# Kernel optimization log

Measured on AMD Instinct MI355X. Metric: run time of the kernel, lower is better.

Reference implementation:

```python
import jax, jax.numpy as jnp
import numpy as np
from jax import lax

N_T, N_CAPS, CAP_DIM = 8, 16, 16
EPS = 1e-6


def setup_inputs() -> dict:
    key = jax.random.key(0)
    k1, k2 = jax.random.split(key)
    B, H, W = 4, 64, 64
    C = N_T * N_CAPS * CAP_DIM  # 2048
    z = jax.random.normal(k1, (B, C, H, W), dtype=jnp.float32)
    u = jax.random.normal(k2, (B, C, H, W), dtype=jnp.float32)
    weight = jnp.ones((1, 1, 3, 3, 1), dtype=jnp.float32)  # Conv3d (O,I,kT,kD,kS), init ones
    beta = jnp.ones((1,), dtype=jnp.float32)  # correlated_mean_beta, mu_init=1.0
    return {"z": z, "u": u, "weight": weight, "beta": beta}


def reference(z, u, weight, beta):
    B, C, H, W = u.shape
    hw = H * W
    # (B, n_t, n_caps, cap_dim, hw) -> (B, n_caps, n_t, cap_dim, hw) -> (B*n_caps, 1, n_t, cap_dim, hw)
    u_caps = u.reshape(B, N_T, N_CAPS, CAP_DIM, hw)
    u_caps = jnp.transpose(u_caps, (0, 2, 1, 3, 4))
    u_caps = u_caps.reshape(-1, 1, N_T, CAP_DIM, hw)
    u_sq = u_caps * u_caps
    # circular pad over transform and cap_dim axes to keep 'same' size with 3x3x1 kernel
    padded = jnp.pad(u_sq, ((0, 0), (0, 0), (1, 1), (1, 1), (0, 0)), mode="wrap")
    v = lax.conv_general_dilated(
        padded, weight, window_strides=(1, 1, 1), padding="VALID",
        dimension_numbers=("NCDHW", "OIDHW", "NCDHW"),
    )  # (B*n_caps, 1, n_t, cap_dim, hw)
    v = v.reshape(B, N_CAPS, N_T, CAP_DIM, hw)
    v = jnp.transpose(v, (0, 2, 1, 3, 4)).reshape(z.shape)
    std = lax.rsqrt(v + EPS)
    s = (z + beta) * std
    return s
```

## Files before the change

### kernel.cpp

```cpp
#include <hip/hip_runtime.h>

#define N_T 8
#define N_CAPS 16
#define CAP_DIM 16
#define HW 4096
#define P_TILE 64
#define EPS 1e-6f

__global__ __launch_bounds__(256) void caps_norm_kernel(
    const float* __restrict__ z, const float* __restrict__ u,
    const float* __restrict__ w, const float* __restrict__ beta,
    float* __restrict__ out)
{
    __shared__ float lds[128 * P_TILE];

    const int tid = threadIdx.x;
    const int bid = blockIdx.x;
    const int ptile = bid & 63;
    const int c     = (bid >> 6) & 15;
    const int b     = bid >> 10;
    const int p0    = ptile * P_TILE;

    float W9[9];
#pragma unroll
    for (int i = 0; i < 9; ++i) W9[i] = w[i];
    const float bet = beta[0];

    const size_t base_b = (size_t)b * 2048 * HW;

#pragma unroll
    for (int k = 0; k < 8; ++k) {
        int s = tid + k * 256;
        int r = s >> 4;
        int q = s & 15;
        int t = r >> 4, d = r & 15;
        int ch = t * 256 + c * 16 + d;
        const float4 v = *(const float4*)(u + base_b + (size_t)ch * HW + p0 + q * 4);
        float4 sq;
        sq.x = v.x * v.x; sq.y = v.y * v.y; sq.z = v.z * v.z; sq.w = v.w * v.w;
        *(float4*)(lds + r * P_TILE + q * 4) = sq;
    }
    __syncthreads();

    const float4* L = (const float4*)lds;

#pragma unroll
    for (int k = 0; k < 8; ++k) {
        int s = tid + k * 256;
        int r = s >> 4;
        int q = s & 15;
        int t = r >> 4, d = r & 15;

        float ax = 0.f, ay = 0.f, az = 0.f, aw = 0.f;
#pragma unroll
        for (int i = 0; i < 3; ++i) {
            int tt = (t + i + 7) & 7;
#pragma unroll
            for (int j = 0; j < 3; ++j) {
                int dd = (d + j + 15) & 15;
                float ww = W9[i * 3 + j];
                float4 a = L[((tt << 4) + dd) * 16 + q];
                ax += ww * a.x; ay += ww * a.y; az += ww * a.z; aw += ww * a.w;
            }
        }

        int ch = t * 256 + c * 16 + d;
        size_t gidx = base_b + (size_t)ch * HW + p0 + q * 4;
        const float4 z4 = *(const float4*)(z + gidx);
        float4 o;
        o.x = (z4.x + bet) * rsqrtf(ax + EPS);
        o.y = (z4.y + bet) * rsqrtf(ay + EPS);
        o.z = (z4.z + bet) * rsqrtf(az + EPS);
        o.w = (z4.w + bet) * rsqrtf(aw + EPS);
        *(float4*)(out + gidx) = o;
    }
}

extern "C" void kernel_launch(void* const* d_in, const int* in_sizes, int n_in,
                              void* d_out, int out_size, void* d_ws, size_t ws_size,
                              hipStream_t stream) {
    const float* z    = (const float*)d_in[0];
    const float* u    = (const float*)d_in[1];
    const float* w    = (const float*)d_in[2];
    const float* beta = (const float*)d_in[3];
    float* out = (float*)d_out;

    caps_norm_kernel<<<dim3(4096), dim3(256), 0, stream>>>(z, u, w, beta, out);
}
```

Measured before the change: 317.7 us.

## Double-buffer LDS and prefetch next tile across four tiles per block

Each block now processes four consecutive pixel tiles instead of one. The u and z loads for the next tile are issued before computing the current tile, and the squared values go into alternating LDS buffers. The aim is to overlap global memory latency with the stencil compute and to amortise the per-block setup. In exchange the grid shrinks by four, LDS use per block doubles and register pressure rises, which can reduce occupancy.

After: 321.2 us. About the same (+1.1%).

```diff
diff --git a/kernel.cpp b/kernel.cpp
--- a/kernel.cpp
+++ b/kernel.cpp
@@ -5,21 +5,22 @@
 #define CAP_DIM 16
 #define HW 4096
 #define P_TILE 64
+#define NTILES 4
 #define EPS 1e-6f
 
-__global__ __launch_bounds__(256) void caps_norm_kernel(
+__global__ __launch_bounds__(256, 2) void caps_norm_kernel(
     const float* __restrict__ z, const float* __restrict__ u,
     const float* __restrict__ w, const float* __restrict__ beta,
     float* __restrict__ out)
 {
-    __shared__ float lds[128 * P_TILE];
+    __shared__ float lds[2][128 * P_TILE];
 
     const int tid = threadIdx.x;
     const int bid = blockIdx.x;
-    const int ptile = bid & 63;
-    const int c     = (bid >> 6) & 15;
-    const int b     = bid >> 10;
-    const int p0    = ptile * P_TILE;
+    const int pg  = bid & 15;
+    const int c   = (bid >> 4) & 15;
+    const int b   = bid >> 8;
+    const int pbase = pg * (P_TILE * NTILES);
 
     float W9[9];
 #pragma unroll
@@ -28,52 +29,95 @@
 
     const size_t base_b = (size_t)b * 2048 * HW;
 
+    int RR[8], QQ[8];
+    size_t GOFF[8];
 #pragma unroll
     for (int k = 0; k < 8; ++k) {
-        int s = tid + k * 256;
-        int r = s >> 4;
-        int q = s & 15;
+        int s = tid + (k << 8);
+        int r = s >> 4, q = s & 15;
         int t = r >> 4, d = r & 15;
         int ch = t * 256 + c * 16 + d;
-        const float4 v = *(const float4*)(u + base_b + (size_t)ch * HW + p0 + q * 4);
-        float4 sq;
-        sq.x = v.x * v.x; sq.y = v.y * v.y; sq.z = v.z * v.z; sq.w = v.w * v.w;
-        *(float4*)(lds + r * P_TILE + q * 4) = sq;
+        RR[k] = r; QQ[k] = q;
+        GOFF[k] = base_b + (size_t)ch * HW + (size_t)(q << 2);
     }
+
+    float4 uN[8], zA[8], zB[8];
+
+#define STAGE_LOAD(TI, ZREG)                                                 \
+    {                                                                        \
+        const int p0_ = pbase + (TI) * P_TILE;                               \
+        _Pragma("unroll")                                                    \
+        for (int k = 0; k < 8; ++k) {                                        \
+            uN[k]   = *(const float4*)(u + GOFF[k] + p0_);                   \
+            ZREG[k] = *(const float4*)(z + GOFF[k] + p0_);                   \
+        }                                                                    \
+    }
+
+#define SQ_WRITE(BUF)                                                        \
+    {                                                                        \
+        _Pragma("unroll")                                                    \
+        for (int k = 0; k < 8; ++k) {                                        \
+            float4 v = uN[k];                                                \
+            float4 sq;                                                       \
+            sq.x = v.x*v.x; sq.y = v.y*v.y; sq.z = v.z*v.z; sq.w = v.w*v.w;  \
+            *(float4*)(&lds[BUF][RR[k] * P_TILE + QQ[k] * 4]) = sq;          \
+        }                                                                    \
+    }
+
+#define COMPUTE(TI, BUF, ZREG)                                               \
+    {                                                                        \
+        const int p0_ = pbase + (TI) * P_TILE;                               \
+        _Pragma("unroll")                                                    \
+        for (int k = 0; k < 8; ++k) {                                        \
+            int r = RR[k], q = QQ[k];                                        \
+            int t = r >> 4, d = r & 15;                                      \
+            float ax = 0.f, ay = 0.f, az = 0.f, aw = 0.f;                    \
+            _Pragma("unroll")                                                \
+            for (int i = 0; i < 3; ++i) {                                    \
+                int tt = (t + i + 7) & 7;                                    \
+                _Pragma("unroll")                                            \
+                for (int j = 0; j < 3; ++j) {                                \
+                    int dd = (d + j + 15) & 15;                              \
+                    float ww = W9[i * 3 + j];                                \
+                    const float4 a = *(const float4*)(                       \
+                        &lds[BUF][((tt << 4) + dd) * P_TILE + q * 4]);       \
+                    ax += ww*a.x; ay += ww*a.y; az += ww*a.z; aw += ww*a.w;  \
+                }                                                            \
+            }                                                                \
+            const float4 z4 = ZREG[k];                                       \
+            float4 o;                                                        \
+            o.x = (z4.x + bet) * rsqrtf(ax + EPS);                           \
+            o.y = (z4.y + bet) * rsqrtf(ay + EPS);                           \
+            o.z = (z4.z + bet) * rsqrtf(az + EPS);                           \
+            o.w = (z4.w + bet) * rsqrtf(aw + EPS);                           \
+            *(float4*)(out + GOFF[k] + p0_) = o;                             \
+        }                                                                    \
+    }
+
+    STAGE_LOAD(0, zA)
+    SQ_WRITE(0)
     __syncthreads();
 
-    const float4* L = (const float4*)lds;
+    STAGE_LOAD(1, zB)
+    COMPUTE(0, 0, zA)
+    SQ_WRITE(1)
+    __syncthreads();
 
-#pragma unroll
-    for (int k = 0; k < 8; ++k) {
-        int s = tid + k * 256;
-        int r = s >> 4;
-        int q = s & 15;
-        int t = r >> 4, d = r & 15;
+    STAGE_LOAD(2, zA)
+    COMPUTE(1, 1, zB)
+    SQ_WRITE(0)
+    __syncthreads();
 
-        float ax = 0.f, ay = 0.f, az = 0.f, aw = 0.f;
-#pragma unroll
-        for (int i = 0; i < 3; ++i) {
-            int tt = (t + i + 7) & 7;
-#pragma unroll
-            for (int j = 0; j < 3; ++j) {
-                int dd = (d + j + 15) & 15;
-                float ww = W9[i * 3 + j];
-                float4 a = L[((tt << 4) + dd) * 16 + q];
-                ax += ww * a.x; ay += ww * a.y; az += ww * a.z; aw += ww * a.w;
-            }
-        }
+    STAGE_LOAD(3, zB)
+    COMPUTE(2, 0, zA)
+    SQ_WRITE(1)
+    __syncthreads();
 
-        int ch = t * 256 + c * 16 + d;
-        size_t gidx = base_b + (size_t)ch * HW + p0 + q * 4;
-        const float4 z4 = *(const float4*)(z + gidx);
-        float4 o;
-        o.x = (z4.x + bet) * rsqrtf(ax + EPS);
-        o.y = (z4.y + bet) * rsqrtf(ay + EPS);
-        o.z = (z4.z + bet) * rsqrtf(az + EPS);
-        o.w = (z4.w + bet) * rsqrtf(aw + EPS);
-        *(float4*)(out + gidx) = o;
-    }
+    COMPUTE(3, 1, zB)
+
+#undef STAGE_LOAD
+#undef SQ_WRITE
+#undef COMPUTE
 }
 
 extern "C" void kernel_launch(void* const* d_in, const int* in_sizes, int n_in,
@@ -85,5 +129,5 @@
     const float* beta = (const float*)d_in[3];
     float* out = (float*)d_out;
 
-    caps_norm_kernel<<<dim3(4096), dim3(256), 0, stream>>>(z, u, w, beta, out);
+    caps_norm_kernel<<<dim3(1024), dim3(256), 0, stream>>>(z, u, w, beta, out);
 }
```

## Replace LDS tiling with register-resident rolling window over transform axis

Applied to the files above, without the earlier changes.

Each thread now owns four pixels of one capsule and keeps three or four transform rows of squared u in registers, stepping through the 8 transforms with a rotating buffer. Loads for the next row are issued while the current row is computed, and the circular wrap row is kept resident. This removes LDS staging and the block barrier. The grid shrinks from 4096 to 256 blocks with heavy register use (launch_bounds 256,1), which risks low occupancy and leaves many CUs idle on a memory-bound kernel.

New measurement: 377.7 us. 18.9% more time.

```diff
diff --git a/kernel.cpp b/kernel.cpp
--- a/kernel.cpp
+++ b/kernel.cpp
@@ -1,79 +1,86 @@
 #include <hip/hip_runtime.h>
 
-#define N_T 8
-#define N_CAPS 16
-#define CAP_DIM 16
 #define HW 4096
-#define P_TILE 64
 #define EPS 1e-6f
 
-__global__ __launch_bounds__(256) void caps_norm_kernel(
+__device__ __forceinline__ void fma4(float4& a, float s, const float4& v) {
+    a.x = fmaf(s, v.x, a.x);
+    a.y = fmaf(s, v.y, a.y);
+    a.z = fmaf(s, v.z, a.z);
+    a.w = fmaf(s, v.w, a.w);
+}
+
+__global__ __launch_bounds__(256, 1) void caps_norm_kernel(
     const float* __restrict__ z, const float* __restrict__ u,
     const float* __restrict__ w, const float* __restrict__ beta,
     float* __restrict__ out)
 {
-    __shared__ float lds[128 * P_TILE];
-
     const int tid = threadIdx.x;
     const int bid = blockIdx.x;
-    const int ptile = bid & 63;
-    const int c     = (bid >> 6) & 15;
-    const int b     = bid >> 10;
-    const int p0    = ptile * P_TILE;
+    const int pg  = bid & 3;
+    const int c   = (bid >> 2) & 15;
+    const int b   = bid >> 6;
+    const int p   = (pg << 10) + (tid << 2);
 
     float W9[9];
 #pragma unroll
     for (int i = 0; i < 9; ++i) W9[i] = w[i];
     const float bet = beta[0];
 
-    const size_t base_b = (size_t)b * 2048 * HW;
+    const size_t base = ((size_t)b * 2048 + (size_t)c * 16) * HW + p;
+    const float* up = u + base;
+    const float* zp = z + base;
+    float*       op = out + base;
 
-#pragma unroll
-    for (int k = 0; k < 8; ++k) {
-        int s = tid + k * 256;
-        int r = s >> 4;
-        int q = s & 15;
-        int t = r >> 4, d = r & 15;
-        int ch = t * 256 + c * 16 + d;
-        const float4 v = *(const float4*)(u + base_b + (size_t)ch * HW + p0 + q * 4);
-        float4 sq;
-        sq.x = v.x * v.x; sq.y = v.y * v.y; sq.z = v.z * v.z; sq.w = v.w * v.w;
-        *(float4*)(lds + r * P_TILE + q * 4) = sq;
+    float4 A[16], B[16], C[16], PIN[16];
+
+#define LOADROW(DST, T)                                                      \
+    _Pragma("unroll")                                                        \
+    for (int d = 0; d < 16; ++d)                                             \
+        DST[d] = *(const float4*)(up + ((T) * 256 + d) * HW);
+
+#define SQR(DST)                                                             \
+    _Pragma("unroll")                                                        \
+    for (int d = 0; d < 16; ++d) {                                           \
+        DST[d].x *= DST[d].x; DST[d].y *= DST[d].y;                          \
+        DST[d].z *= DST[d].z; DST[d].w *= DST[d].w;                          \
     }
-    __syncthreads();
 
-    const float4* L = (const float4*)lds;
+#define COMP(T, W0, W1, W2)                                                  \
+    _Pragma("unroll")                                                        \
+    for (int d = 0; d < 16; ++d) {                                           \
+        const int dm = (d + 15) & 15, dp = (d + 1) & 15;                     \
+        const float4 z4 = *(const float4*)(zp + ((T) * 256 + d) * HW);       \
+        float4 acc = make_float4(0.f, 0.f, 0.f, 0.f);                        \
+        fma4(acc, W9[0], W0[dm]); fma4(acc, W9[1], W0[d]); fma4(acc, W9[2], W0[dp]); \
+        fma4(acc, W9[3], W1[dm]); fma4(acc, W9[4], W1[d]); fma4(acc, W9[5], W1[dp]); \
+        fma4(acc, W9[6], W2[dm]); fma4(acc, W9[7], W2[d]); fma4(acc, W9[8], W2[dp]); \
+        float4 o;                                                            \
+        o.x = (z4.x + bet) * rsqrtf(acc.x + EPS);                            \
+        o.y = (z4.y + bet) * rsqrtf(acc.y + EPS);                            \
+        o.z = (z4.z + bet) * rsqrtf(acc.z + EPS);                            \
+        o.w = (z4.w + bet) * rsqrtf(acc.w + EPS);                            \
+        *(float4*)(op + ((T) * 256 + d) * HW) = o;                           \
+    }
 
-#pragma unroll
-    for (int k = 0; k < 8; ++k) {
-        int s = tid + k * 256;
-        int r = s >> 4;
-        int q = s & 15;
-        int t = r >> 4, d = r & 15;
+    LOADROW(A, 7)
+    LOADROW(PIN, 0)
+    LOADROW(B, 1)
+    LOADROW(C, 2)
+    SQR(A) SQR(PIN)
 
-        float ax = 0.f, ay = 0.f, az = 0.f, aw = 0.f;
-#pragma unroll
-        for (int i = 0; i < 3; ++i) {
-            int tt = (t + i + 7) & 7;
-#pragma unroll
-            for (int j = 0; j < 3; ++j) {
-                int dd = (d + j + 15) & 15;
-                float ww = W9[i * 3 + j];
-                float4 a = L[((tt << 4) + dd) * 16 + q];
-                ax += ww * a.x; ay += ww * a.y; az += ww * a.z; aw += ww * a.w;
-            }
-        }
+    SQR(B)  COMP(0, A, PIN, B)  LOADROW(A, 3)
+    SQR(C)  COMP(1, PIN, B, C)
+    SQR(A)  COMP(2, B, C, A)    LOADROW(B, 4)
+    SQR(B)  COMP(3, C, A, B)    LOADROW(C, 5)
+    SQR(C)  COMP(4, A, B, C)    LOADROW(A, 6)
+    SQR(A)  COMP(5, B, C, A)    LOADROW(B, 7)
+    SQR(B)  COMP(6, C, A, B)
+            COMP(7, A, B, PIN)
 
-        int ch = t * 256 + c * 16 + d;
-        size_t gidx = base_b + (size_t)ch * HW + p0 + q * 4;
-        const float4 z4 = *(const float4*)(z + gidx);
-        float4 o;
-        o.x = (z4.x + bet) * rsqrtf(ax + EPS);
-        o.y = (z4.y + bet) * rsqrtf(ay + EPS);
-        o.z = (z4.z + bet) * rsqrtf(az + EPS);
-        o.w = (z4.w + bet) * rsqrtf(aw + EPS);
-        *(float4*)(out + gidx) = o;
-    }
+#undef LOADROW
+#undef SQR
+#undef COMP
 }
 
 extern "C" void kernel_launch(void* const* d_in, const int* in_sizes, int n_in,
@@ -85,5 +92,5 @@
     const float* beta = (const float*)d_in[3];
     float* out = (float*)d_out;
 
-    caps_norm_kernel<<<dim3(4096), dim3(256), 0, stream>>>(z, u, w, beta, out);
+    caps_norm_kernel<<<dim3(256), dim3(256), 0, stream>>>(z, u, w, beta, out);
 }
```
